# Optimization experiments

Measured on AMD Instinct MI355X. Metric: run time of the kernel, lower is better.

Reference implementation:

```python
import jax, jax.numpy as jnp
import numpy as np

B, L, D = 8, 4096, 768   # batch, seq_len, embedding_dim
E, K, H = 8, 2, 1536     # num_experts, top_k_experts, expert hidden (proj_factor=2)


def setup_inputs() -> dict:
    key = jax.random.key(0)
    k0, k1, k2, k3, k4 = jax.random.split(key, 5)
    s_in = 1.0 / np.sqrt(D).astype(np.float32)
    s_out = 1.0 / np.sqrt(H).astype(np.float32)
    return {
        "hidden_states": jax.random.normal(k0, (B, L, D), jnp.float32),
        "scores": jax.random.normal(k1, (B, L, E), jnp.float32),
        "W1": jax.random.normal(k2, (E, D, H), jnp.float32) * s_in,
        "Wg": jax.random.normal(k3, (E, D, H), jnp.float32) * s_in,
        "W2": jax.random.normal(k4, (E, H, D), jnp.float32) * s_out,
    }


def reference(hidden_states, scores, W1, Wg, W2):
    # Router: top-k over experts, softmax over the selected k scores.
    topk_scores, topk_idx = jax.lax.top_k(scores, K)          # (B,L,K)
    w = jax.nn.softmax(topk_scores, axis=-1)                  # (B,L,K)
    # Combine weights per expert: sum_k w_k * [topk_idx_k == e] -> (B,L,E).
    # (top_k returns distinct indices, matching the torch one_hot accumulation.)
    comb = jnp.einsum("blk,blke->ble", w, jax.nn.one_hot(topk_idx, E, dtype=w.dtype))
    # Expert = gated up-projection (mLSTM-style SiLU-free gate) + down-projection.
    out = jnp.zeros_like(hidden_states)
    for e in range(E):  # fixed small expert count; data dims stay vectorized
        h = (hidden_states @ W1[e]) * jax.nn.sigmoid(hidden_states @ Wg[e])  # (B,L,H)
        out = out + comb[..., e, None] * (h @ W2[e])                          # (B,L,D)
    return out
```

## Files before the change

kernel.cpp:

```cpp
#include <hip/hip_runtime.h>
#include <hip/hip_bf16.h>

#define NB 8
#define NL 4096
#define ND 768
#define NE 8
#define NK 2
#define NH 1536
#define NTOK (NB*NL)
#define NPAIR (NTOK*NK)
#define BM 128
#define BN 128
#define BK 64
#define ROWTILES 520
#define PADN (ROWTILES*BM)

typedef __attribute__((ext_vector_type(8))) short bf16x8;
typedef __attribute__((ext_vector_type(4))) float f32x4;

static __device__ __forceinline__ unsigned short f2bf(float f) {
    union { float f; unsigned int u; } v; v.f = f;
    unsigned int r = v.u + 0x7fffu + ((v.u >> 16) & 1u);
    return (unsigned short)(r >> 16);
}

static __device__ __forceinline__ void gload16(const unsigned short* g, unsigned short* l) {
    __builtin_amdgcn_global_load_lds(
        (const __attribute__((address_space(1))) void*)g,
        (__attribute__((address_space(3))) void*)l, 16, 0, 0);
}

__global__ void router_kernel(const float* __restrict__ scores,
                              int* __restrict__ counts,
                              int* __restrict__ te, float* __restrict__ tw) {
    int t = blockIdx.x * 256 + threadIdx.x;
    if (t >= NTOK) return;
    float s[NE];
#pragma unroll
    for (int e = 0; e < NE; ++e) s[e] = scores[t * NE + e];
    int i0 = 0; float m0 = s[0];
#pragma unroll
    for (int e = 1; e < NE; ++e) if (s[e] > m0) { m0 = s[e]; i0 = e; }
    int i1 = -1; float m1 = -1e30f;
#pragma unroll
    for (int e = 0; e < NE; ++e) if (e != i0 && s[e] > m1) { m1 = s[e]; i1 = e; }
    float z = expf(m1 - m0);
    float inv = 1.f / (1.f + z);
    te[t * 2 + 0] = i0; te[t * 2 + 1] = i1;
    tw[t * 2 + 0] = inv; tw[t * 2 + 1] = z * inv;
    atomicAdd(&counts[i0], 1);
    atomicAdd(&counts[i1], 1);
}

__global__ void scan_kernel(const int* __restrict__ counts,
                            int* __restrict__ offsets, int* __restrict__ cursors) {
    if (threadIdx.x == 0) {
        int off = 0;
        for (int e = 0; e < NE; ++e) {
            offsets[e] = off;
            cursors[e] = off;
            off += ((counts[e] + BM - 1) / BM) * BM;
        }
        offsets[NE] = off;
    }
}

__global__ void fill_kernel(const int* __restrict__ te, const float* __restrict__ tw,
                            int* __restrict__ cursors,
                            int* __restrict__ ptok, float* __restrict__ pw) {
    int t = blockIdx.x * 256 + threadIdx.x;
    if (t >= NTOK) return;
#pragma unroll
    for (int k = 0; k < NK; ++k) {
        int e = te[t * 2 + k];
        int pos = atomicAdd(&cursors[e], 1);
        ptok[pos] = t;
        pw[pos] = tw[t * 2 + k];
    }
}

__global__ void cvt_kernel(const float* __restrict__ src, unsigned short* __restrict__ dst, int n8) {
    int i = blockIdx.x * 256 + threadIdx.x;
    if (i >= n8) return;
    const float4* p = (const float4*)(src + (size_t)i * 8);
    float4 a = p[0], b = p[1];
    uint4 v;
    v.x = f2bf(a.x) | ((unsigned)f2bf(a.y) << 16);
    v.y = f2bf(a.z) | ((unsigned)f2bf(a.w) << 16);
    v.z = f2bf(b.x) | ((unsigned)f2bf(b.y) << 16);
    v.w = f2bf(b.z) | ((unsigned)f2bf(b.w) << 16);
    *(uint4*)(dst + (size_t)i * 8) = v;
}

__global__ void tcvt_kernel(const float* __restrict__ src, unsigned short* __restrict__ dst,
                            int R, int C) {
    __shared__ float t[32][33];
    int e = blockIdx.z;
    const float* s = src + (size_t)e * R * C;
    unsigned short* d = dst + (size_t)e * R * C;
    int c0 = blockIdx.x * 32, r0 = blockIdx.y * 32;
    int tx = threadIdx.x & 31, ty4 = (threadIdx.x >> 5) * 4;
#pragma unroll
    for (int i = 0; i < 4; ++i)
        t[ty4 + i][tx] = s[(size_t)(r0 + ty4 + i) * C + c0 + tx];
    __syncthreads();
#pragma unroll
    for (int i = 0; i < 4; ++i)
        d[(size_t)(c0 + ty4 + i) * R + r0 + tx] = f2bf(t[tx][ty4 + i]);
}

template<bool PRE>
__global__ __launch_bounds__(256, 2) void gemm1_kernel(
    const float* __restrict__ hidden, const unsigned short* __restrict__ hidbf,
    const float* __restrict__ W1, const float* __restrict__ Wg,
    const unsigned short* __restrict__ W1t, const unsigned short* __restrict__ Wgt,
    const unsigned short* __restrict__ zbuf,
    const int* __restrict__ offsets, const int* __restrict__ ptok,
    const float* __restrict__ pw, unsigned short* __restrict__ hbuf, int tile0)
{
    __shared__ unsigned short lA[BM * BK];
    __shared__ unsigned short lB1[BN * BK];
    __shared__ unsigned short lBg[BN * BK];

    const int tid = threadIdx.x;
    const int lane = tid & 63;
    const int wid = tid >> 6;
    const int wr = wid >> 1, wc = wid & 1;
    const int row0 = (tile0 + blockIdx.x) * BM;
    const int rowbase = tile0 * BM;
    const int col0 = blockIdx.y * BN;

    int e = 0;
#pragma unroll
    for (int i = 1; i < NE; ++i) e += (row0 >= offsets[i]) ? 1 : 0;
    const size_t wbase = (size_t)e * ND * NH;

    f32x4 acc1[4][4], accg[4][4];
#pragma unroll
    for (int m = 0; m < 4; ++m)
#pragma unroll
        for (int n = 0; n < 4; ++n) {
            acc1[m][n] = (f32x4){0.f, 0.f, 0.f, 0.f};
            accg[m][n] = (f32x4){0.f, 0.f, 0.f, 0.f};
        }

    if (PRE) {
        const int lr = lane >> 3;
        const int csw = (lane & 7) ^ lr;
        const unsigned short* gA[4];
        const unsigned short* gB1[4];
        const unsigned short* gBg[4];
#pragma unroll
        for (int i = 0; i < 4; ++i) {
            int r = wid * 32 + i * 8 + lr;
            int tok = ptok[row0 + r];
            gA[i] = (tok >= 0 ? hidbf + (size_t)tok * ND : zbuf) + csw * 8;
            int c = col0 + r;
            gB1[i] = W1t + wbase + (size_t)c * ND + csw * 8;
            gBg[i] = Wgt + wbase + (size_t)c * ND + csw * 8;
        }
        for (int k0 = 0; k0 < ND; k0 += BK) {
#pragma unroll
            for (int i = 0; i < 4; ++i) {
                gload16(gA[i] + k0, &lA[(wid * 32 + i * 8) * BK]);
                gload16(gB1[i] + k0, &lB1[(wid * 32 + i * 8) * BK]);
                gload16(gBg[i] + k0, &lBg[(wid * 32 + i * 8) * BK]);
            }
            __syncthreads();
#pragma unroll
            for (int kk = 0; kk < 2; ++kk) {
                bf16x8 af[4], bfrag[4];
#pragma unroll
                for (int m = 0; m < 4; ++m) {
                    int r = wr * 64 + m * 16 + (lane & 15);
                    int ch = kk * 4 + (lane >> 4);
                    af[m] = *(const bf16x8*)&lA[r * BK + ((ch ^ (r & 7)) * 8)];
                }
#pragma unroll
                for (int n = 0; n < 4; ++n) {
                    int c = wc * 64 + n * 16 + (lane & 15);
                    int ch = kk * 4 + (lane >> 4);
                    bfrag[n] = *(const bf16x8*)&lB1[c * BK + ((ch ^ (c & 7)) * 8)];
                }
#pragma unroll
                for (int m = 0; m < 4; ++m)
#pragma unroll
                    for (int n = 0; n < 4; ++n)
                        acc1[m][n] = __builtin_amdgcn_mfma_f32_16x16x32_bf16(af[m], bfrag[n], acc1[m][n], 0, 0, 0);
#pragma unroll
                for (int n = 0; n < 4; ++n) {
                    int c = wc * 64 + n * 16 + (lane & 15);
                    int ch = kk * 4 + (lane >> 4);
                    bfrag[n] = *(const bf16x8*)&lBg[c * BK + ((ch ^ (c & 7)) * 8)];
                }
#pragma unroll
                for (int m = 0; m < 4; ++m)
#pragma unroll
                    for (int n = 0; n < 4; ++n)
                        accg[m][n] = __builtin_amdgcn_mfma_f32_16x16x32_bf16(af[m], bfrag[n], accg[m][n], 0, 0, 0);
            }
            __syncthreads();
        }
    } else {
        const int sr = tid >> 1;
        const int sck = (tid & 1) * 4;
        const int stok = ptok[row0 + sr];
        const int gcolB = col0 + sr;
        for (int k0 = 0; k0 < ND; k0 += BK) {
#pragma unroll
            for (int i = 0; i < 4; ++i) {
                int ck = sck + i;
                uint4 v;
                if (stok >= 0) {
                    const float4* p = (const float4*)(hidden + (size_t)stok * ND + k0 + ck * 8);
                    float4 f0 = p[0], f1 = p[1];
                    v.x = f2bf(f0.x) | ((unsigned)f2bf(f0.y) << 16);
                    v.y = f2bf(f0.z) | ((unsigned)f2bf(f0.w) << 16);
                    v.z = f2bf(f1.x) | ((unsigned)f2bf(f1.y) << 16);
                    v.w = f2bf(f1.z) | ((unsigned)f2bf(f1.w) << 16);
                } else v = make_uint4(0u, 0u, 0u, 0u);
                *(uint4*)&lA[sr * BK + ((ck ^ (sr & 7)) * 8)] = v;
            }
#pragma unroll
            for (int i = 0; i < 4; ++i) {
                int ck = sck + i;
                const float* bp1 = W1 + wbase + (size_t)(k0 + ck * 8) * NH + gcolB;
                const float* bpg = Wg + wbase + (size_t)(k0 + ck * 8) * NH + gcolB;
                uint4 v1, vg;
                v1.x = f2bf(bp1[0 * NH]) | ((unsigned)f2bf(bp1[1 * NH]) << 16);
                v1.y = f2bf(bp1[2 * NH]) | ((unsigned)f2bf(bp1[3 * NH]) << 16);
                v1.z = f2bf(bp1[4 * NH]) | ((unsigned)f2bf(bp1[5 * NH]) << 16);
                v1.w = f2bf(bp1[6 * NH]) | ((unsigned)f2bf(bp1[7 * NH]) << 16);
                vg.x = f2bf(bpg[0 * NH]) | ((unsigned)f2bf(bpg[1 * NH]) << 16);
                vg.y = f2bf(bpg[2 * NH]) | ((unsigned)f2bf(bpg[3 * NH]) << 16);
                vg.z = f2bf(bpg[4 * NH]) | ((unsigned)f2bf(bpg[5 * NH]) << 16);
                vg.w = f2bf(bpg[6 * NH]) | ((unsigned)f2bf(bpg[7 * NH]) << 16);
                int sidx = sr * BK + ((ck ^ (sr & 7)) * 8);
                *(uint4*)&lB1[sidx] = v1;
                *(uint4*)&lBg[sidx] = vg;
            }
            __syncthreads();
#pragma unroll
            for (int kk = 0; kk < 2; ++kk) {
                bf16x8 af[4], bfrag[4];
#pragma unroll
                for (int m = 0; m < 4; ++m) {
                    int r = wr * 64 + m * 16 + (lane & 15);
                    int ch = kk * 4 + (lane >> 4);
                    af[m] = *(const bf16x8*)&lA[r * BK + ((ch ^ (r & 7)) * 8)];
                }
#pragma unroll
                for (int n = 0; n < 4; ++n) {
                    int c = wc * 64 + n * 16 + (lane & 15);
                    int ch = kk * 4 + (lane >> 4);
                    bfrag[n] = *(const bf16x8*)&lB1[c * BK + ((ch ^ (c & 7)) * 8)];
                }
#pragma unroll
                for (int m = 0; m < 4; ++m)
#pragma unroll
                    for (int n = 0; n < 4; ++n)
                        acc1[m][n] = __builtin_amdgcn_mfma_f32_16x16x32_bf16(af[m], bfrag[n], acc1[m][n], 0, 0, 0);
#pragma unroll
                for (int n = 0; n < 4; ++n) {
                    int c = wc * 64 + n * 16 + (lane & 15);
                    int ch = kk * 4 + (lane >> 4);
                    bfrag[n] = *(const bf16x8*)&lBg[c * BK + ((ch ^ (c & 7)) * 8)];
                }
#pragma unroll
                for (int m = 0; m < 4; ++m)
#pragma unroll
                    for (int n = 0; n < 4; ++n)
                        accg[m][n] = __builtin_amdgcn_mfma_f32_16x16x32_bf16(af[m], bfrag[n], accg[m][n], 0, 0, 0);
            }
            __syncthreads();
        }
    }

#pragma unroll
    for (int m = 0; m < 4; ++m) {
#pragma unroll
        for (int rr = 0; rr < 4; ++rr) {
            int row = wr * 64 + m * 16 + (lane >> 4) * 4 + rr;
            int grow = row0 + row;
            float wt = pw[grow];
            size_t hb = (size_t)(grow - rowbase) * NH + col0;
#pragma unroll
            for (int n = 0; n < 4; ++n) {
                int col = wc * 64 + n * 16 + (lane & 15);
                float x = acc1[m][n][rr];
                float g = accg[m][n][rr];
                float hv = x * (1.f / (1.f + __expf(-g))) * wt;
                hbuf[hb + col] = f2bf(hv);
            }
        }
    }
}

template<bool PRE>
__global__ __launch_bounds__(256, 2) void gemm2_kernel(
    const unsigned short* __restrict__ hbuf, const float* __restrict__ W2,
    const unsigned short* __restrict__ W2t,
    const int* __restrict__ offsets, const int* __restrict__ ptok,
    float* __restrict__ out, int tile0)
{
    __shared__ unsigned short lA[BM * BK];
    __shared__ unsigned short lB[BN * BK];

    const int tid = threadIdx.x;
    const int lane = tid & 63;
    const int wid = tid >> 6;
    const int wr = wid >> 1, wc = wid & 1;
    const int row0 = (tile0 + blockIdx.x) * BM;
    const int rowbase = tile0 * BM;
    const int col0 = blockIdx.y * BN;

    int e = 0;
#pragma unroll
    for (int i = 1; i < NE; ++i) e += (row0 >= offsets[i]) ? 1 : 0;
    const size_t wbase = (size_t)e * NH * ND;

    f32x4 acc[4][4];
#pragma unroll
    for (int m = 0; m < 4; ++m)
#pragma unroll
        for (int n = 0; n < 4; ++n) acc[m][n] = (f32x4){0.f, 0.f, 0.f, 0.f};

    if (PRE) {
        const int lr = lane >> 3;
        const int csw = (lane & 7) ^ lr;
        const unsigned short* gA[4];
        const unsigned short* gB[4];
#pragma unroll
        for (int i = 0; i < 4; ++i) {
            int r = wid * 32 + i * 8 + lr;
            gA[i] = hbuf + (size_t)(row0 - rowbase + r) * NH + csw * 8;
            gB[i] = W2t + wbase + (size_t)(col0 + r) * NH + csw * 8;
        }
        for (int k0 = 0; k0 < NH; k0 += BK) {
#pragma unroll
            for (int i = 0; i < 4; ++i) {
                gload16(gA[i] + k0, &lA[(wid * 32 + i * 8) * BK]);
                gload16(gB[i] + k0, &lB[(wid * 32 + i * 8) * BK]);
            }
            __syncthreads();
#pragma unroll
            for (int kk = 0; kk < 2; ++kk) {
                bf16x8 af[4], bfrag[4];
#pragma unroll
                for (int m = 0; m < 4; ++m) {
                    int r = wr * 64 + m * 16 + (lane & 15);
                    int ch = kk * 4 + (lane >> 4);
                    af[m] = *(const bf16x8*)&lA[r * BK + ((ch ^ (r & 7)) * 8)];
                }
#pragma unroll
                for (int n = 0; n < 4; ++n) {
                    int c = wc * 64 + n * 16 + (lane & 15);
                    int ch = kk * 4 + (lane >> 4);
                    bfrag[n] = *(const bf16x8*)&lB[c * BK + ((ch ^ (c & 7)) * 8)];
                }
#pragma unroll
                for (int m = 0; m < 4; ++m)
#pragma unroll
                    for (int n = 0; n < 4; ++n)
                        acc[m][n] = __builtin_amdgcn_mfma_f32_16x16x32_bf16(af[m], bfrag[n], acc[m][n], 0, 0, 0);
            }
            __syncthreads();
        }
    } else {
        const int sr = tid >> 1;
        const int sck = (tid & 1) * 4;
        const int gcolB = col0 + sr;
        for (int k0 = 0; k0 < NH; k0 += BK) {
#pragma unroll
            for (int i = 0; i < 4; ++i) {
                int ck = sck + i;
                uint4 v = *(const uint4*)(hbuf + (size_t)(row0 - rowbase + sr) * NH + k0 + ck * 8);
                *(uint4*)&lA[sr * BK + ((ck ^ (sr & 7)) * 8)] = v;
            }
#pragma unroll
            for (int i = 0; i < 4; ++i) {
                int ck = sck + i;
                const float* bp = W2 + wbase + (size_t)(k0 + ck * 8) * ND + gcolB;
                uint4 v;
                v.x = f2bf(bp[0 * ND]) | ((unsigned)f2bf(bp[1 * ND]) << 16);
                v.y = f2bf(bp[2 * ND]) | ((unsigned)f2bf(bp[3 * ND]) << 16);
                v.z = f2bf(bp[4 * ND]) | ((unsigned)f2bf(bp[5 * ND]) << 16);
                v.w = f2bf(bp[6 * ND]) | ((unsigned)f2bf(bp[7 * ND]) << 16);
                *(uint4*)&lB[sr * BK + ((ck ^ (sr & 7)) * 8)] = v;
            }
            __syncthreads();
#pragma unroll
            for (int kk = 0; kk < 2; ++kk) {
                bf16x8 af[4], bfrag[4];
#pragma unroll
                for (int m = 0; m < 4; ++m) {
                    int r = wr * 64 + m * 16 + (lane & 15);
                    int ch = kk * 4 + (lane >> 4);
                    af[m] = *(const bf16x8*)&lA[r * BK + ((ch ^ (r & 7)) * 8)];
                }
#pragma unroll
                for (int n = 0; n < 4; ++n) {
                    int c = wc * 64 + n * 16 + (lane & 15);
                    int ch = kk * 4 + (lane >> 4);
                    bfrag[n] = *(const bf16x8*)&lB[c * BK + ((ch ^ (c & 7)) * 8)];
                }
#pragma unroll
                for (int m = 0; m < 4; ++m)
#pragma unroll
                    for (int n = 0; n < 4; ++n)
                        acc[m][n] = __builtin_amdgcn_mfma_f32_16x16x32_bf16(af[m], bfrag[n], acc[m][n], 0, 0, 0);
            }
            __syncthreads();
        }
    }

#pragma unroll
    for (int m = 0; m < 4; ++m) {
#pragma unroll
        for (int rr = 0; rr < 4; ++rr) {
            int row = wr * 64 + m * 16 + (lane >> 4) * 4 + rr;
            int grow = row0 + row;
            int tok = ptok[grow];
            if (tok < 0) continue;
            float* op = out + (size_t)tok * ND + col0;
#pragma unroll
            for (int n = 0; n < 4; ++n) {
                int col = wc * 64 + n * 16 + (lane & 15);
                atomicAdd(op + col, acc[m][n][rr]);
            }
        }
    }
}

extern "C" void kernel_launch(void* const* d_in, const int* in_sizes, int n_in,
                              void* d_out, int out_size, void* d_ws, size_t ws_size,
                              hipStream_t stream) {
    const float* hidden = (const float*)d_in[0];
    const float* scores = (const float*)d_in[1];
    const float* W1 = (const float*)d_in[2];
    const float* Wg = (const float*)d_in[3];
    const float* W2 = (const float*)d_in[4];
    float* out = (float*)d_out;

    char* wsb = (char*)d_ws;
    int* counts = (int*)(wsb + 0);
    int* cursors = (int*)(wsb + 64);
    int* offsets = (int*)(wsb + 128);
    unsigned short* zbuf = (unsigned short*)(wsb + 256);
    int* te = (int*)(wsb + 2048);
    float* tw = (float*)(wsb + 2048 + (size_t)NTOK * 2 * 4);
    int* ptok = (int*)(wsb + 2048 + (size_t)NTOK * 2 * 8);
    float* pw = (float*)(wsb + 2048 + (size_t)NTOK * 2 * 8 + (size_t)PADN * 4);
    size_t fixed = 2048 + (size_t)NTOK * 2 * 8 + (size_t)PADN * 8;
    fixed = (fixed + 255) & ~(size_t)255;

    const size_t hidbf_b = (size_t)NTOK * ND * 2;
    const size_t wt_b    = (size_t)NE * ND * NH * 2;
    const size_t wtot_b  = hidbf_b + 3 * wt_b;

    unsigned short* hidbf = (unsigned short*)(wsb + fixed);
    unsigned short* W1t = (unsigned short*)(wsb + fixed + hidbf_b);
    unsigned short* Wgt = (unsigned short*)(wsb + fixed + hidbf_b + wt_b);
    unsigned short* W2t = (unsigned short*)(wsb + fixed + hidbf_b + 2 * wt_b);

    const int gcand[12] = {1, 2, 3, 4, 6, 8, 13, 26, 52, 104, 260, 520};
    bool pre = false;
    int tiles_pg = 1;
    unsigned short* hbuf = nullptr;
    for (int i = 0; i < 12; ++i) {
        int tpg = (ROWTILES + gcand[i] - 1) / gcand[i];
        size_t hb = (size_t)tpg * BM * NH * 2;
        if (fixed + wtot_b + hb <= ws_size) { pre = true; tiles_pg = tpg; break; }
    }
    if (pre) {
        hbuf = (unsigned short*)(wsb + fixed + wtot_b);
    } else {
        for (int i = 0; i < 12; ++i) {
            int tpg = (ROWTILES + gcand[i] - 1) / gcand[i];
            size_t hb = (size_t)tpg * BM * NH * 2;
            if (fixed + hb <= ws_size) { tiles_pg = tpg; break; }
            tiles_pg = 1;
        }
        hbuf = (unsigned short*)(wsb + fixed);
    }

    hipMemsetAsync(counts, 0, 256, stream);
    hipMemsetAsync(zbuf, 0, 1536 + 256, stream);
    hipMemsetAsync(ptok, 0xFF, (size_t)PADN * 4, stream);
    hipMemsetAsync(pw, 0, (size_t)PADN * 4, stream);
    hipMemsetAsync(out, 0, (size_t)out_size * 4, stream);

    router_kernel<<<NTOK / 256, 256, 0, stream>>>(scores, counts, te, tw);
    scan_kernel<<<1, 64, 0, stream>>>(counts, offsets, cursors);
    fill_kernel<<<NTOK / 256, 256, 0, stream>>>(te, tw, cursors, ptok, pw);

    if (pre) {
        cvt_kernel<<<(NTOK * ND / 8 + 255) / 256, 256, 0, stream>>>(hidden, hidbf, NTOK * ND / 8);
        dim3 tg1(NH / 32, ND / 32, NE);
        tcvt_kernel<<<tg1, 256, 0, stream>>>(W1, W1t, ND, NH);
        tcvt_kernel<<<tg1, 256, 0, stream>>>(Wg, Wgt, ND, NH);
        dim3 tg2(ND / 32, NH / 32, NE);
        tcvt_kernel<<<tg2, 256, 0, stream>>>(W2, W2t, NH, ND);
    }

    for (int t0 = 0; t0 < ROWTILES; t0 += tiles_pg) {
        int nt = ROWTILES - t0 < tiles_pg ? ROWTILES - t0 : tiles_pg;
        dim3 g1(nt, NH / BN);
        dim3 g2(nt, ND / BN);
        if (pre) {
            gemm1_kernel<true><<<g1, 256, 0, stream>>>(hidden, hidbf, W1, Wg, W1t, Wgt, zbuf,
                                                       offsets, ptok, pw, hbuf, t0);
            gemm2_kernel<true><<<g2, 256, 0, stream>>>(hbuf, W2, W2t, offsets, ptok, out, t0);
        } else {
            gemm1_kernel<false><<<g1, 256, 0, stream>>>(hidden, hidbf, W1, Wg, W1t, Wgt, zbuf,
                                                        offsets, ptok, pw, hbuf, t0);
            gemm2_kernel<false><<<g2, 256, 0, stream>>>(hbuf, W2, W2t, offsets, ptok, out, t0);
        }
    }
}
```

Baseline: 1.431 ms.

## Replace atomic scatter in down-projection with per-pair partial buffer and combine kernel

Gemm2 now writes each routed pair's output row to a dense partial buffer, in fp32 or bf16 depending on workspace size, instead of doing float atomicAdds into the token output. A new combine kernel sums the two partials per token using a recorded pair-position map, which also removes the output memset. The row-tile group size is fixed to 130 tiles when the partial buffer fits, and launch bounds are raised to 3 blocks per CU for both GEMMs. The trade-off is extra workspace, an extra write and read pass over the partials, and possible register spills from the tighter occupancy bound.

```diff
diff --git a/kernel.cpp b/kernel.cpp
--- a/kernel.cpp
+++ b/kernel.cpp
@@ -23,6 +23,10 @@
     unsigned int r = v.u + 0x7fffu + ((v.u >> 16) & 1u);
     return (unsigned short)(r >> 16);
 }
+static __device__ __forceinline__ float bf2f(unsigned short b) {
+    union { unsigned int u; float f; } v; v.u = ((unsigned)b) << 16;
+    return v.f;
+}
 
 static __device__ __forceinline__ void gload16(const unsigned short* g, unsigned short* l) {
     __builtin_amdgcn_global_load_lds(
@@ -67,7 +71,8 @@
 
 __global__ void fill_kernel(const int* __restrict__ te, const float* __restrict__ tw,
                             int* __restrict__ cursors,
-                            int* __restrict__ ptok, float* __restrict__ pw) {
+                            int* __restrict__ ptok, float* __restrict__ pw,
+                            int* __restrict__ pairpos) {
     int t = blockIdx.x * 256 + threadIdx.x;
     if (t >= NTOK) return;
 #pragma unroll
@@ -76,6 +81,7 @@
         int pos = atomicAdd(&cursors[e], 1);
         ptok[pos] = t;
         pw[pos] = tw[t * 2 + k];
+        pairpos[t * 2 + k] = pos;
     }
 }
 
@@ -110,7 +116,7 @@
 }
 
 template<bool PRE>
-__global__ __launch_bounds__(256, 2) void gemm1_kernel(
+__global__ __launch_bounds__(256, 3) void gemm1_kernel(
     const float* __restrict__ hidden, const unsigned short* __restrict__ hidbf,
     const float* __restrict__ W1, const float* __restrict__ Wg,
     const unsigned short* __restrict__ W1t, const unsigned short* __restrict__ Wgt,
@@ -296,12 +302,13 @@
     }
 }
 
-template<bool PRE>
-__global__ __launch_bounds__(256, 2) void gemm2_kernel(
+template<bool PRE, int PART>
+__global__ __launch_bounds__(256, 3) void gemm2_kernel(
     const unsigned short* __restrict__ hbuf, const float* __restrict__ W2,
     const unsigned short* __restrict__ W2t,
     const int* __restrict__ offsets, const int* __restrict__ ptok,
-    float* __restrict__ out, int tile0)
+    float* __restrict__ out, unsigned short* __restrict__ part16,
+    float* __restrict__ part32, int tile0)
 {
     __shared__ unsigned short lA[BM * BK];
     __shared__ unsigned short lB[BN * BK];
@@ -420,16 +427,66 @@
         for (int rr = 0; rr < 4; ++rr) {
             int row = wr * 64 + m * 16 + (lane >> 4) * 4 + rr;
             int grow = row0 + row;
-            int tok = ptok[grow];
-            if (tok < 0) continue;
-            float* op = out + (size_t)tok * ND + col0;
-#pragma unroll
-            for (int n = 0; n < 4; ++n) {
-                int col = wc * 64 + n * 16 + (lane & 15);
-                atomicAdd(op + col, acc[m][n][rr]);
-            }
-        }
-    }
+            if (PART == 0) {
+                int tok = ptok[grow];
+                if (tok < 0) continue;
+                float* op = out + (size_t)tok * ND + col0;
+#pragma unroll
+                for (int n = 0; n < 4; ++n) {
+                    int col = wc * 64 + n * 16 + (lane & 15);
+                    atomicAdd(op + col, acc[m][n][rr]);
+                }
+            } else if (PART == 1) {
+                unsigned short* pp = part16 + (size_t)grow * ND + col0;
+#pragma unroll
+                for (int n = 0; n < 4; ++n) {
+                    int col = wc * 64 + n * 16 + (lane & 15);
+                    pp[col] = f2bf(acc[m][n][rr]);
+                }
+            } else {
+                float* pp = part32 + (size_t)grow * ND + col0;
+#pragma unroll
+                for (int n = 0; n < 4; ++n) {
+                    int col = wc * 64 + n * 16 + (lane & 15);
+                    pp[col] = acc[m][n][rr];
+                }
+            }
+        }
+    }
+}
+
+__global__ void combine16_kernel(const unsigned short* __restrict__ part,
+                                 const int* __restrict__ pairpos, float* __restrict__ out) {
+    int i = blockIdx.x * 256 + threadIdx.x;
+    int t = i / (ND / 8), ch = i % (ND / 8);
+    int p0 = pairpos[t * 2], p1 = pairpos[t * 2 + 1];
+    uint4 a = *(const uint4*)(part + (size_t)p0 * ND + ch * 8);
+    uint4 b = *(const uint4*)(part + (size_t)p1 * ND + ch * 8);
+    float4 o0, o1;
+    o0.x = bf2f((unsigned short)(a.x)) + bf2f((unsigned short)(b.x));
+    o0.y = bf2f((unsigned short)(a.x >> 16)) + bf2f((unsigned short)(b.x >> 16));
+    o0.z = bf2f((unsigned short)(a.y)) + bf2f((unsigned short)(b.y));
+    o0.w = bf2f((unsigned short)(a.y >> 16)) + bf2f((unsigned short)(b.y >> 16));
+    o1.x = bf2f((unsigned short)(a.z)) + bf2f((unsigned short)(b.z));
+    o1.y = bf2f((unsigned short)(a.z >> 16)) + bf2f((unsigned short)(b.z >> 16));
+    o1.z = bf2f((unsigned short)(a.w)) + bf2f((unsigned short)(b.w));
+    o1.w = bf2f((unsigned short)(a.w >> 16)) + bf2f((unsigned short)(b.w >> 16));
+    float4* op = (float4*)(out + (size_t)t * ND + ch * 8);
+    op[0] = o0; op[1] = o1;
+}
+
+__global__ void combine32_kernel(const float* __restrict__ part,
+                                 const int* __restrict__ pairpos, float* __restrict__ out) {
+    int i = blockIdx.x * 256 + threadIdx.x;
+    int t = i / (ND / 8), ch = i % (ND / 8);
+    int p0 = pairpos[t * 2], p1 = pairpos[t * 2 + 1];
+    const float4* a = (const float4*)(part + (size_t)p0 * ND + ch * 8);
+    const float4* b = (const float4*)(part + (size_t)p1 * ND + ch * 8);
+    float4 a0 = a[0], a1 = a[1], b0 = b[0], b1 = b[1];
+    float4 o0 = {a0.x + b0.x, a0.y + b0.y, a0.z + b0.z, a0.w + b0.w};
+    float4 o1 = {a1.x + b1.x, a1.y + b1.y, a1.z + b1.z, a1.w + b1.w};
+    float4* op = (float4*)(out + (size_t)t * ND + ch * 8);
+    op[0] = o0; op[1] = o1;
 }
 
 extern "C" void kernel_launch(void* const* d_in, const int* in_sizes, int n_in,
@@ -451,48 +508,73 @@
     float* tw = (float*)(wsb + 2048 + (size_t)NTOK * 2 * 4);
     int* ptok = (int*)(wsb + 2048 + (size_t)NTOK * 2 * 8);
     float* pw = (float*)(wsb + 2048 + (size_t)NTOK * 2 * 8 + (size_t)PADN * 4);
-    size_t fixed = 2048 + (size_t)NTOK * 2 * 8 + (size_t)PADN * 8;
+    int* pairpos = (int*)(wsb + 2048 + (size_t)NTOK * 2 * 8 + (size_t)PADN * 8);
+    size_t fixed = 2048 + (size_t)NTOK * 2 * 8 + (size_t)PADN * 8 + (size_t)NTOK * 2 * 4;
     fixed = (fixed + 255) & ~(size_t)255;
 
     const size_t hidbf_b = (size_t)NTOK * ND * 2;
     const size_t wt_b    = (size_t)NE * ND * NH * 2;
     const size_t wtot_b  = hidbf_b + 3 * wt_b;
+    const size_t part16_b = (size_t)PADN * ND * 2;
+    const size_t part32_b = (size_t)PADN * ND * 4;
 
     unsigned short* hidbf = (unsigned short*)(wsb + fixed);
     unsigned short* W1t = (unsigned short*)(wsb + fixed + hidbf_b);
     unsigned short* Wgt = (unsigned short*)(wsb + fixed + hidbf_b + wt_b);
     unsigned short* W2t = (unsigned short*)(wsb + fixed + hidbf_b + 2 * wt_b);
 
-    const int gcand[12] = {1, 2, 3, 4, 6, 8, 13, 26, 52, 104, 260, 520};
+    int partmode = -1, tiles_pg = 1;
     bool pre = false;
-    int tiles_pg = 1;
+    unsigned short* part16 = nullptr;
+    float* part32 = nullptr;
     unsigned short* hbuf = nullptr;
-    for (int i = 0; i < 12; ++i) {
-        int tpg = (ROWTILES + gcand[i] - 1) / gcand[i];
-        size_t hb = (size_t)tpg * BM * NH * 2;
-        if (fixed + wtot_b + hb <= ws_size) { pre = true; tiles_pg = tpg; break; }
-    }
-    if (pre) {
-        hbuf = (unsigned short*)(wsb + fixed + wtot_b);
-    } else {
+
+    {
+        const int pmc[4] = {2, 1, 1, 1};
+        const int tpc[4] = {130, 130, 52, 26};
+        for (int i = 0; i < 4; ++i) {
+            size_t pb = (pmc[i] == 2) ? part32_b : part16_b;
+            size_t hb = (size_t)tpc[i] * BM * NH * 2;
+            if (fixed + wtot_b + pb + hb <= ws_size) {
+                partmode = pmc[i]; tiles_pg = tpc[i]; pre = true;
+                part16 = (unsigned short*)(wsb + fixed + wtot_b);
+                part32 = (float*)(wsb + fixed + wtot_b);
+                hbuf = (unsigned short*)(wsb + fixed + wtot_b + pb);
+                break;
+            }
+        }
+    }
+    if (partmode < 0) {
+        partmode = 0;
+        const int gcand[12] = {1, 2, 3, 4, 6, 8, 13, 26, 52, 104, 260, 520};
         for (int i = 0; i < 12; ++i) {
             int tpg = (ROWTILES + gcand[i] - 1) / gcand[i];
             size_t hb = (size_t)tpg * BM * NH * 2;
-            if (fixed + hb <= ws_size) { tiles_pg = tpg; break; }
-            tiles_pg = 1;
-        }
-        hbuf = (unsigned short*)(wsb + fixed);
+            if (fixed + wtot_b + hb <= ws_size) { pre = true; tiles_pg = tpg; break; }
+        }
+        if (pre) {
+            hbuf = (unsigned short*)(wsb + fixed + wtot_b);
+        } else {
+            for (int i = 0; i < 12; ++i) {
+                int tpg = (ROWTILES + gcand[i] - 1) / gcand[i];
+                size_t hb = (size_t)tpg * BM * NH * 2;
+                if (fixed + hb <= ws_size) { tiles_pg = tpg; break; }
+                tiles_pg = 1;
+            }
+            hbuf = (unsigned short*)(wsb + fixed);
+        }
     }
 
     hipMemsetAsync(counts, 0, 256, stream);
     hipMemsetAsync(zbuf, 0, 1536 + 256, stream);
     hipMemsetAsync(ptok, 0xFF, (size_t)PADN * 4, stream);
     hipMemsetAsync(pw, 0, (size_t)PADN * 4, stream);
-    hipMemsetAsync(out, 0, (size_t)out_size * 4, stream);
+    if (partmode == 0)
+        hipMemsetAsync(out, 0, (size_t)out_size * 4, stream);
 
     router_kernel<<<NTOK / 256, 256, 0, stream>>>(scores, counts, te, tw);
     scan_kernel<<<1, 64, 0, stream>>>(counts, offsets, cursors);
-    fill_kernel<<<NTOK / 256, 256, 0, stream>>>(te, tw, cursors, ptok, pw);
+    fill_kernel<<<NTOK / 256, 256, 0, stream>>>(te, tw, cursors, ptok, pw, pairpos);
 
     if (pre) {
         cvt_kernel<<<(NTOK * ND / 8 + 255) / 256, 256, 0, stream>>>(hidden, hidbf, NTOK * ND / 8);
@@ -510,11 +592,21 @@
         if (pre) {
             gemm1_kernel<true><<<g1, 256, 0, stream>>>(hidden, hidbf, W1, Wg, W1t, Wgt, zbuf,
                                                        offsets, ptok, pw, hbuf, t0);
-            gemm2_kernel<true><<<g2, 256, 0, stream>>>(hbuf, W2, W2t, offsets, ptok, out, t0);
+            if (partmode == 2)
+                gemm2_kernel<true, 2><<<g2, 256, 0, stream>>>(hbuf, W2, W2t, offsets, ptok, out, part16, part32, t0);
+            else if (partmode == 1)
+                gemm2_kernel<true, 1><<<g2, 256, 0, stream>>>(hbuf, W2, W2t, offsets, ptok, out, part16, part32, t0);
+            else
+                gemm2_kernel<true, 0><<<g2, 256, 0, stream>>>(hbuf, W2, W2t, offsets, ptok, out, part16, part32, t0);
         } else {
             gemm1_kernel<false><<<g1, 256, 0, stream>>>(hidden, hidbf, W1, Wg, W1t, Wgt, zbuf,
                                                         offsets, ptok, pw, hbuf, t0);
-            gemm2_kernel<false><<<g2, 256, 0, stream>>>(hbuf, W2, W2t, offsets, ptok, out, t0);
-        }
-    }
-}
+            gemm2_kernel<false, 0><<<g2, 256, 0, stream>>>(hbuf, W2, W2t, offsets, ptok, out, part16, part32, t0);
+        }
+    }
+
+    if (partmode == 1)
+        combine16_kernel<<<NTOK * (ND / 8) / 256, 256, 0, stream>>>(part16, pairpos, out);
+    else if (partmode == 2)
+        combine32_kernel<<<NTOK * (ND / 8) / 256, 256, 0, stream>>>(part32, pairpos, out);
+}
```

After: 2.206 ms. 1.54x slower.
